# Performance work log

Measured on AMD Instinct MI355X. Metric: run time of the kernel, lower is better.

Reference implementation:

```python
import jax, jax.numpy as jnp
import numpy as np

B, N, D = 256, 64, 256   # graphs, nodes/graph, hidden dim (node_size*extend_dim)
T, E = B * N, 524288     # total nodes, total edges
NODE, BOND, K = 128, 16, 3
RRELU_SLOPE = (1.0 / 8.0 + 1.0 / 3.0) / 2.0  # eval-mode RReLU slope


def rrelu(x):
    return jnp.where(x >= 0, x, RRELU_SLOPE * x)


def conv_step(x, src, dst, ea, Wn, We, bm, Ws, bs):
    # message on each edge, scatter-add to destination, self-transform + update
    msg = jax.nn.relu(x[src] @ Wn + ea @ We + bm)          # [E, D]
    agg = jax.ops.segment_sum(msg, dst, num_segments=T)    # [T, D]
    return jax.nn.relu(x @ Ws + agg + bs)


def readout(x):
    # GlobalPool: cat([mean, sum, sort_pool(k=3)], -1) -> [B, 5D]
    xr = x.reshape(B, N, D)
    mean, s = xr.mean(1), xr.sum(1)
    order = jnp.argsort(-xr[..., -1], axis=1)[:, :K]                      # [B, K]
    topk = jnp.take_along_axis(xr, order[..., None], axis=1).reshape(B, K * D)
    return jnp.concatenate([mean, s, topk], -1)


def dot_pool(x1, x2):
    # per-graph cross-molecule dot product, max & mean -> [B, 2]
    item = jnp.einsum('bnd,bmd->bnm', x1.reshape(B, N, D), x2.reshape(B, N, D))
    return jnp.stack([item.max((1, 2)), item.mean((1, 2))], -1)


def setup_inputs() -> dict:
    key = jax.random.key(0)
    ks = jax.random.split(key, 32)
    batch = jnp.repeat(jnp.arange(B, dtype=jnp.int64), N)
    off = jnp.repeat(jnp.arange(B, dtype=jnp.int64) * N, E // B)

    def edges(k):
        s = jax.random.randint(k, (2, E), 0, N).astype(jnp.int64) + off[None, :]
        return s

    def w(k, shape):
        fan = shape[0]
        return jax.random.normal(k, shape, jnp.float32) * (1.0 / np.sqrt(fan))

    return {
        'x1': jax.random.normal(ks[0], (T, NODE), jnp.float32),
        'edge_index1': edges(ks[1]),
        'edge_attr1': jax.random.normal(ks[2], (E, BOND), jnp.float32),
        'batch1': batch,
        'x2': jax.random.normal(ks[3], (T, NODE), jnp.float32),
        'edge_index2': edges(ks[4]),
        'edge_attr2': jax.random.normal(ks[5], (E, BOND), jnp.float32),
        'batch2': batch,
        'W0_1': w(ks[6], (NODE, D)), 'b0_1': jnp.zeros(D),
        'W0_2': w(ks[7], (NODE, D)), 'b0_2': jnp.zeros(D),
        'Wn1': w(ks[8], (D, D)), 'We1': w(ks[9], (BOND, D)), 'bm1': jnp.zeros(D),
        'Ws1': w(ks[10], (D, D)), 'bs1': jnp.zeros(D),
        'Wn2': w(ks[11], (D, D)), 'We2': w(ks[12], (BOND, D)), 'bm2': jnp.zeros(D),
        'Ws2': w(ks[13], (D, D)), 'bs2': jnp.zeros(D),
        'Wf1': w(ks[14], (5 * D, D)), 'bf1': jnp.zeros(D),
        'Wf2': w(ks[15], (5 * D, D)), 'bf2': jnp.zeros(D),
        'Wo1': w(ks[16], (2 * D + 6, D)), 'bo1': jnp.zeros(D),
        'Wo2': w(ks[17], (D, 2)), 'bo2': jnp.zeros(2),
    }


def reference(x1, edge_index1, edge_attr1, batch1, x2, edge_index2, edge_attr2, batch2,
              W0_1, b0_1, W0_2, b0_2,
              Wn1, We1, bm1, Ws1, bs1,
              Wn2, We2, bm2, Ws2, bs2,
              Wf1, bf1, Wf2, bf2, Wo1, bo1, Wo2, bo2):
    xm1 = rrelu(x1 @ W0_1 + b0_1)
    xm2 = rrelu(x2 @ W0_2 + b0_2)
    s1, d1 = edge_index1[0], edge_index1[1]
    s2, d2 = edge_index2[0], edge_index2[1]
    fusion = []
    for _ in range(3):  # message_steps
        xm1 = conv_step(xm1, s1, d1, edge_attr1, Wn1, We1, bm1, Ws1, bs1)
        xm2 = conv_step(xm2, s2, d2, edge_attr2, Wn2, We2, bm2, Ws2, bs2)
        fusion.append(dot_pool(xm1, xm2))
    outm1 = readout(xm1) @ Wf1 + bf1
    outm2 = readout(xm2) @ Wf2 + bf2
    out = jnp.concatenate([outm1, outm2, jnp.concatenate(fusion, -1)], -1)
    out = out @ Wo1 + bo1
    return out @ Wo2 + bo2
```

## Files before the change

### kernel.cpp

```cpp
#include <hip/hip_runtime.h>
#include <hip/hip_fp16.h>

#define E_TOTAL 524288
#define RRELU_SLOPE 0.22916666666666666f

typedef float f32x4 __attribute__((ext_vector_type(4)));
typedef short short8_t __attribute__((ext_vector_type(8)));
typedef _Float16 half4_t __attribute__((ext_vector_type(4)));
typedef _Float16 h2v __attribute__((ext_vector_type(2)));

#define MFMA16F16 __builtin_amdgcn_mfma_f32_16x16x16f16

#if defined(__HIP_DEVICE_COMPILE__)
# if __has_builtin(__builtin_amdgcn_cvt_pkrtz)
#  define HAVE_PKRTZ 1
# endif
#endif

__device__ inline unsigned short f2bf(float x) {
  unsigned int u = __float_as_uint(x);
  u += 0x7FFFu + ((u >> 16) & 1u);
  return (unsigned short)(u >> 16);
}

__device__ inline unsigned int pack_h2(float a, float b) {
  __half2 h = __floats2half2_rn(a, b);
  return __builtin_bit_cast(unsigned int, h);
}

__device__ inline unsigned int pack_h2_fast(float a, float b) {
#ifdef HAVE_PKRTZ
  return __builtin_bit_cast(unsigned int, __builtin_amdgcn_cvt_pkrtz(a, b));
#else
  return pack_h2(a, b);
#endif
}

__global__ __launch_bounds__(256) void gemm_bf16_dual(
    const float* __restrict__ A1, const unsigned short* __restrict__ BT1,
    const float* __restrict__ bias1, float* __restrict__ C1,
    unsigned short* __restrict__ Ch1,
    const float* __restrict__ A2, const unsigned short* __restrict__ BT2,
    const float* __restrict__ bias2, float* __restrict__ C2,
    unsigned short* __restrict__ Ch2,
    int lda, int ldc, int K, int act)
{
  const float* A = blockIdx.z ? A2 : A1;
  const unsigned short* BT = blockIdx.z ? BT2 : BT1;
  const float* bias = blockIdx.z ? bias2 : bias1;
  float* C = blockIdx.z ? C2 : C1;
  unsigned short* Ch = blockIdx.z ? Ch2 : Ch1;

  __shared__ unsigned short As[128][32];
  __shared__ unsigned short Bs[128][32];
  const int tid = threadIdx.x;
  const int bm = blockIdx.x, bn = blockIdx.y;
  const int w = tid >> 6, l = tid & 63;
  const int wm = (w & 1) * 64, wn = (w >> 1) * 64;
  const int q = l >> 4, r = l & 15;

  f32x4 acc[4][4];
  for (int i = 0; i < 4; ++i)
    for (int j = 0; j < 4; ++j)
      acc[i][j] = (f32x4){0.f, 0.f, 0.f, 0.f};

  const int sm = tid >> 1;
  const int sk = (tid & 1) * 16;
  const float* ap = A + (size_t)(bm * 128 + sm) * lda + sk;
  const unsigned short* bp = BT + (size_t)(bn * 128 + sm) * K + sk;

  for (int k0 = 0; k0 < K; k0 += 32) {
    float4 f0 = *(const float4*)(ap + k0);
    float4 f1 = *(const float4*)(ap + k0 + 4);
    float4 f2 = *(const float4*)(ap + k0 + 8);
    float4 f3 = *(const float4*)(ap + k0 + 12);
    uint4 p0, p1;
    p0.x = (unsigned)f2bf(f0.x) | ((unsigned)f2bf(f0.y) << 16);
    p0.y = (unsigned)f2bf(f0.z) | ((unsigned)f2bf(f0.w) << 16);
    p0.z = (unsigned)f2bf(f1.x) | ((unsigned)f2bf(f1.y) << 16);
    p0.w = (unsigned)f2bf(f1.z) | ((unsigned)f2bf(f1.w) << 16);
    p1.x = (unsigned)f2bf(f2.x) | ((unsigned)f2bf(f2.y) << 16);
    p1.y = (unsigned)f2bf(f2.z) | ((unsigned)f2bf(f2.w) << 16);
    p1.z = (unsigned)f2bf(f3.x) | ((unsigned)f2bf(f3.y) << 16);
    p1.w = (unsigned)f2bf(f3.z) | ((unsigned)f2bf(f3.w) << 16);
    *(uint4*)&As[sm][sk] = p0;
    *(uint4*)&As[sm][sk + 8] = p1;
    uint4 b0 = *(const uint4*)(bp + k0);
    uint4 b1 = *(const uint4*)(bp + k0 + 8);
    *(uint4*)&Bs[sm][sk] = b0;
    *(uint4*)&Bs[sm][sk + 8] = b1;
    __syncthreads();

    short8_t af[4], bfr[4];
    for (int mt = 0; mt < 4; ++mt)
      af[mt] = *(const short8_t*)&As[wm + mt * 16 + r][q * 8];
    for (int nt = 0; nt < 4; ++nt)
      bfr[nt] = *(const short8_t*)&Bs[wn + nt * 16 + r][q * 8];
    for (int mt = 0; mt < 4; ++mt)
      for (int nt = 0; nt < 4; ++nt)
        acc[mt][nt] = __builtin_amdgcn_mfma_f32_16x16x32_bf16(
            af[mt], bfr[nt], acc[mt][nt], 0, 0, 0);
    __syncthreads();
  }

  for (int nt = 0; nt < 4; ++nt) {
    int gc = bn * 128 + wn + nt * 16 + r;
    float bv = bias ? bias[gc] : 0.f;
    for (int mt = 0; mt < 4; ++mt) {
      int gm = bm * 128 + wm + mt * 16 + q * 4;
      for (int rr = 0; rr < 4; ++rr) {
        float v = acc[mt][nt][rr] + bv;
        if (act == 2) v = (v >= 0.f) ? v : v * RRELU_SLOPE;
        if (Ch) Ch[(size_t)(gm + rr) * ldc + gc] = f2bf(v);
        else    C[(size_t)(gm + rr) * ldc + gc] = v;
      }
    }
  }
}

__global__ __launch_bounds__(256) void gemm_h_dual(
    const unsigned short* __restrict__ Ah1, const unsigned short* __restrict__ BT1,
    const float* __restrict__ bias1, float* __restrict__ C1,
    const unsigned short* __restrict__ Ah2, const unsigned short* __restrict__ BT2,
    const float* __restrict__ bias2, float* __restrict__ C2,
    int ldc, int K)
{
  const unsigned short* A = blockIdx.z ? Ah2 : Ah1;
  const unsigned short* BT = blockIdx.z ? BT2 : BT1;
  const float* bias = blockIdx.z ? bias2 : bias1;
  float* C = blockIdx.z ? C2 : C1;

  __shared__ unsigned short As[128][32];
  __shared__ unsigned short Bs[128][32];
  const int tid = threadIdx.x;
  const int bm = blockIdx.x, bn = blockIdx.y;
  const int w = tid >> 6, l = tid & 63;
  const int wm = (w & 1) * 64, wn = (w >> 1) * 64;
  const int q = l >> 4, r = l & 15;

  f32x4 acc[4][4];
  for (int i = 0; i < 4; ++i)
    for (int j = 0; j < 4; ++j)
      acc[i][j] = (f32x4){0.f, 0.f, 0.f, 0.f};

  const int sm = tid >> 1;
  const int sk = (tid & 1) * 16;
  const unsigned short* ap = A + (size_t)(bm * 128 + sm) * K + sk;
  const unsigned short* bp = BT + (size_t)(bn * 128 + sm) * K + sk;

  for (int k0 = 0; k0 < K; k0 += 32) {
    uint4 a0 = *(const uint4*)(ap + k0);
    uint4 a1 = *(const uint4*)(ap + k0 + 8);
    uint4 b0 = *(const uint4*)(bp + k0);
    uint4 b1 = *(const uint4*)(bp + k0 + 8);
    *(uint4*)&As[sm][sk] = a0;
    *(uint4*)&As[sm][sk + 8] = a1;
    *(uint4*)&Bs[sm][sk] = b0;
    *(uint4*)&Bs[sm][sk + 8] = b1;
    __syncthreads();

    short8_t af[4], bfr[4];
    for (int mt = 0; mt < 4; ++mt)
      af[mt] = *(const short8_t*)&As[wm + mt * 16 + r][q * 8];
    for (int nt = 0; nt < 4; ++nt)
      bfr[nt] = *(const short8_t*)&Bs[wn + nt * 16 + r][q * 8];
    for (int mt = 0; mt < 4; ++mt)
      for (int nt = 0; nt < 4; ++nt)
        acc[mt][nt] = __builtin_amdgcn_mfma_f32_16x16x32_bf16(
            af[mt], bfr[nt], acc[mt][nt], 0, 0, 0);
    __syncthreads();
  }

  for (int nt = 0; nt < 4; ++nt) {
    int gc = bn * 128 + wn + nt * 16 + r;
    float bv = bias ? bias[gc] : 0.f;
    for (int mt = 0; mt < 4; ++mt) {
      int gm = bm * 128 + wm + mt * 16 + q * 4;
      for (int rr = 0; rr < 4; ++rr)
        C[(size_t)(gm + rr) * ldc + gc] = acc[mt][nt][rr] + bv;
    }
  }
}

__global__ __launch_bounds__(256) void sort_edges_dual(
    const int* __restrict__ ei1, const int* __restrict__ ei2,
    int* __restrict__ meta1, int* __restrict__ meta2,
    int* __restrict__ perm1, int* __restrict__ perm2,
    int* __restrict__ starts1, int* __restrict__ starts2)
{
  const int mol = blockIdx.x >> 8;
  const int g = blockIdx.x & 255;
  const int* eidx = mol ? ei2 : ei1;
  int* meta = mol ? meta2 : meta1;
  int* perm = mol ? perm2 : perm1;
  int* starts = mol ? starts2 : starts1;

  __shared__ int cnt[4][64];
  __shared__ int startS[65];
  __shared__ int cur[64];
  const int t = threadIdx.x, w = t >> 6;
  cnt[w][t & 63] = 0;
  if (t < 64) cur[t] = 0;
  __syncthreads();
  for (int i = t; i < 2048; i += 256)
    atomicAdd(&cnt[w][eidx[E_TOTAL + g * 2048 + i] & 63], 1);
  __syncthreads();
  if (t == 0) {
    int acc = 0;
    for (int n = 0; n < 64; ++n) {
      startS[n] = acc;
      acc += cnt[0][n] + cnt[1][n] + cnt[2][n] + cnt[3][n];
    }
    startS[64] = acc;
  }
  __syncthreads();
  if (t < 65) starts[g * 65 + t] = startS[t];
  for (int i = t; i < 2048; i += 256) {
    int s = eidx[g * 2048 + i] & 63;
    int d = eidx[E_TOTAL + g * 2048 + i] & 63;
    int p = startS[d] + atomicAdd(&cur[d], 1);
    meta[g * 2048 + p] = s | (d << 8);
    perm[g * 2048 + p] = i;
  }
}

__global__ __launch_bounds__(256) void ea_gather_pack_dual(
    const float* __restrict__ ea1, const float* __restrict__ ea2,
    const int* __restrict__ perm1, const int* __restrict__ perm2,
    unsigned int* __restrict__ o1, unsigned int* __restrict__ o2)
{
  const int mol = blockIdx.x >> 11;
  const float* ea = mol ? ea2 : ea1;
  const int* perm = mol ? perm2 : perm1;
  unsigned int* out = mol ? o2 : o1;
  int p = (blockIdx.x & 2047) * 256 + threadIdx.x;
  int g = p >> 11;
  int i = perm[p];
  const float* s = ea + (size_t)(g * 2048 + i) * 16;
  float4 v0 = *(const float4*)(s);
  float4 v1 = *(const float4*)(s + 4);
  float4 v2 = *(const float4*)(s + 8);
  float4 v3 = *(const float4*)(s + 12);
  uint4 q0, q1;
  q0.x = pack_h2(v0.x, v0.y); q0.y = pack_h2(v0.z, v0.w);
  q0.z = pack_h2(v1.x, v1.y); q0.w = pack_h2(v1.z, v1.w);
  q1.x = pack_h2(v2.x, v2.y); q1.y = pack_h2(v2.z, v2.w);
  q1.z = pack_h2(v3.x, v3.y); q1.w = pack_h2(v3.z, v3.w);
  *(uint4*)(out + (size_t)p * 8) = q0;
  *(uint4*)(out + (size_t)p * 8 + 4) = q1;
}

__global__ __launch_bounds__(512, 4) void edge_conv_dual(
    const float* __restrict__ y1, const int* __restrict__ meta1,
    const unsigned int* __restrict__ eas1, const unsigned int* __restrict__ wep1,
    const int* __restrict__ st1, float* __restrict__ xo1,
    unsigned short* __restrict__ xoh1,
    const float* __restrict__ y2, const int* __restrict__ meta2,
    const unsigned int* __restrict__ eas2, const unsigned int* __restrict__ wep2,
    const int* __restrict__ st2, float* __restrict__ xo2,
    unsigned short* __restrict__ xoh2)
{
  const float* y; const int* meta; const unsigned int* eas;
  const unsigned int* wep; const int* st; float* xo; unsigned short* xoh;
  if (blockIdx.z == 0) { y = y1; meta = meta1; eas = eas1; wep = wep1; st = st1; xo = xo1; xoh = xoh1; }
  else                 { y = y2; meta = meta2; eas = eas2; wep = wep2; st = st2; xo = xo2; xoh = xoh2; }

  __shared__ unsigned int ypk[4160];
  const int g = blockIdx.x >> 1;
  const int dbase = (blockIdx.x & 1) * 128;
  const int tid = threadIdx.x;
  const int l = tid & 63;
  const int w = tid >> 6;
  const int rh = l & 15;
  const int qh = l >> 4;
  const int rhw = w * 8 + rh;

  for (int i = tid; i < 4096; i += 512) {
    int n = i >> 6, j = i & 63;
    const float* yr = y + (size_t)(g * 64 + n) * 512 + dbase + j;
    ypk[n * 65 + j] = pack_h2_fast(yr[0], yr[64]);
  }

  uint2 bfr[8];
#pragma unroll
  for (int c = 0; c < 8; ++c) {
    int d = dbase + c * 16 + rh;
    bfr[c].x = wep[(2 * qh) * 256 + d];
    bfr[c].y = wep[(2 * qh + 1) * 256 + d];
  }

  __syncthreads();

  const int estart = st[g * 65 + w * 8];
  const int eend   = st[g * 65 + w * 8 + 8];

  f32x4 acc[8];
#pragma unroll
  for (int i = 0; i < 8; ++i) acc[i] = (f32x4){0.f, 0.f, 0.f, 0.f};

  int base = estart;
  uint2 af = {0u, 0u};
  int mv = -1;
  if (base < eend) {
    int lim = eend - base; if (lim > 16) lim = 16;
    af = *(const uint2*)(eas + ((size_t)g * 2048 + base + (rh < lim ? rh : lim - 1)) * 8 + 2 * qh);
    int m = meta[(size_t)g * 2048 + base + (l < lim ? l : lim - 1)];
    mv = (l < lim) ? m : -1;
  }

  while (base < eend) {
    int mp[4];
#pragma unroll
    for (int v = 0; v < 4; ++v)
      mp[v] = __builtin_amdgcn_ds_bpermute(qh * 16 + v * 4, mv);

    int nbase = base + 16;
    uint2 afn = af;
    int mvn = -1;
    if (nbase < eend) {
      int nlim = eend - nbase; if (nlim > 16) nlim = 16;
      afn = *(const uint2*)(eas + ((size_t)g * 2048 + nbase + (rh < nlim ? rh : nlim - 1)) * 8 + 2 * qh);
      int m2 = meta[(size_t)g * 2048 + nbase + (l < nlim ? l : nlim - 1)];
      mvn = (l < nlim) ? m2 : -1;
    }

    half4_t afh = __builtin_bit_cast(half4_t, af);
    f32x4 pa[4], pb[4];
#pragma unroll
    for (int cp = 0; cp < 4; ++cp) {
      f32x4 z = (f32x4){0.f, 0.f, 0.f, 0.f};
      pa[cp] = MFMA16F16(afh, __builtin_bit_cast(half4_t, bfr[cp]), z, 0, 0, 0);
      pb[cp] = MFMA16F16(afh, __builtin_bit_cast(half4_t, bfr[cp + 4]), z, 0, 0, 0);
    }

    unsigned int yv[4][4];
    unsigned int ind[4];
#pragma unroll
    for (int v = 0; v < 4; ++v) {
      int sv = mp[v] & 63;
      int dv = (mp[v] >> 8) & 255;
      const unsigned int* yb = ypk + sv * 65 + rh;
      yv[0][v] = yb[0];
      yv[1][v] = yb[16];
      yv[2][v] = yb[32];
      yv[3][v] = yb[48];
      ind[v] = (dv == rhw) ? 0x3C00u : 0u;
    }
    uint2 su;
    su.x = ind[0] | (ind[1] << 16);
    su.y = ind[2] | (ind[3] << 16);
    half4_t sfrag = __builtin_bit_cast(half4_t, su);

    const h2v hz = {(_Float16)0.0f, (_Float16)0.0f};
#pragma unroll
    for (int cp = 0; cp < 4; ++cp) {
      unsigned int t[4];
#pragma unroll
      for (int v = 0; v < 4; ++v) {
        h2v s = __builtin_bit_cast(h2v, pack_h2_fast(pa[cp][v], pb[cp][v]));
        s = s + __builtin_bit_cast(h2v, yv[cp][v]);
        s = __builtin_elementwise_max(s, hz);
        t[v] = __builtin_bit_cast(unsigned int, s);
      }
      uint2 blo, bhi;
      blo.x = __builtin_amdgcn_perm(t[1], t[0], 0x05040100u);
      blo.y = __builtin_amdgcn_perm(t[3], t[2], 0x05040100u);
      bhi.x = __builtin_amdgcn_perm(t[1], t[0], 0x07060302u);
      bhi.y = __builtin_amdgcn_perm(t[3], t[2], 0x07060302u);
      acc[cp]     = MFMA16F16(sfrag, __builtin_bit_cast(half4_t, blo), acc[cp], 0, 0, 0);
      acc[cp + 4] = MFMA16F16(sfrag, __builtin_bit_cast(half4_t, bhi), acc[cp + 4], 0, 0, 0);
    }

    base = nbase;
    af = afn;
    mv = mvn;
  }

  if (qh < 2) {
#pragma unroll
    for (int v = 0; v < 4; ++v) {
      int node = g * 64 + w * 8 + qh * 4 + v;
      const float* ysp = y + (size_t)node * 512 + 256 + dbase + rh;
      float* xop = xo + (size_t)node * 256 + dbase + rh;
      unsigned short* xohp = xoh + (size_t)node * 256 + dbase + rh;
#pragma unroll
      for (int cp = 0; cp < 8; ++cp) {
        int dim = (cp & 3) * 16 + (cp >> 2) * 64;
        float val = fmaxf(ysp[dim] + acc[cp][v], 0.f);
        xop[dim] = val;
        xohp[dim] = f2bf(val);
      }
    }
  }
}

__global__ __launch_bounds__(256) void dot_pool_mfma(
    const unsigned short* __restrict__ x1h, const unsigned short* __restrict__ x2h,
    float* __restrict__ fusion, int step)
{
  __shared__ unsigned short s1[64][256];
  __shared__ unsigned short s2[64][256];
  const int g = blockIdx.x, tid = threadIdx.x;
  const int l = tid & 63, w = tid >> 6;
  const int r = l & 15, q = l >> 4;

  for (int i = tid; i < 2048; i += 256) {
    int row = i >> 5, c = i & 31;
    int cs = c ^ (row & 7);
    *(uint4*)&s1[row][cs * 8] = *(const uint4*)(x1h + (size_t)(g * 64 + row) * 256 + c * 8);
    *(uint4*)&s2[row][cs * 8] = *(const uint4*)(x2h + (size_t)(g * 64 + row) * 256 + c * 8);
  }
  __syncthreads();

  const int m0 = w * 16;
  const int sx = r & 7;
  f32x4 acc[4];
#pragma unroll
  for (int nt = 0; nt < 4; ++nt) acc[nt] = (f32x4){0.f, 0.f, 0.f, 0.f};

#pragma unroll
  for (int kb = 0; kb < 32; kb += 4) {
    int ch = (kb + q) ^ sx;
    short8_t af = *(const short8_t*)&s1[m0 + r][ch * 8];
#pragma unroll
    for (int nt = 0; nt < 4; ++nt) {
      short8_t bf = *(const short8_t*)&s2[nt * 16 + r][ch * 8];
      acc[nt] = __builtin_amdgcn_mfma_f32_16x16x32_bf16(af, bf, acc[nt], 0, 0, 0);
    }
  }

  float mymax = -1e30f, mysum = 0.f;
#pragma unroll
  for (int nt = 0; nt < 4; ++nt)
#pragma unroll
    for (int reg = 0; reg < 4; ++reg) {
      float v = acc[nt][reg];
      mymax = fmaxf(mymax, v);
      mysum += v;
    }
  for (int off = 32; off; off >>= 1) {
    mymax = fmaxf(mymax, __shfl_down(mymax, off, 64));
    mysum += __shfl_down(mysum, off, 64);
  }
  __syncthreads();
  float* red = (float*)&s1[0][0];
  if (l == 0) { red[w] = mymax; red[8 + w] = mysum; }
  __syncthreads();
  if (tid == 0) {
    float gm = fmaxf(fmaxf(red[0], red[1]), fmaxf(red[2], red[3]));
    float gs = red[8] + red[9] + red[10] + red[11];
    fusion[g * 6 + step * 2] = gm;
    fusion[g * 6 + step * 2 + 1] = gs * (1.f / 4096.f);
  }
}

__global__ __launch_bounds__(256) void readout_dual(
    const float* __restrict__ xm1, const float* __restrict__ xm2,
    float* __restrict__ R1, float* __restrict__ R2)
{
  const int mol = blockIdx.x >> 8;
  const float* xm = mol ? xm2 : xm1;
  float* R = mol ? R2 : R1;
  __shared__ float lastcol[64];
  __shared__ int topi[3];
  const int g = blockIdx.x & 255, d = threadIdx.x;
  float s = 0.f;
  for (int n = 0; n < 64; ++n) s += xm[(size_t)(g * 64 + n) * 256 + d];
  R[(size_t)g * 1280 + d] = s * (1.f / 64.f);
  R[(size_t)g * 1280 + 256 + d] = s;
  if (d < 64) lastcol[d] = xm[(size_t)(g * 64 + d) * 256 + 255];
  __syncthreads();
  if (d == 0) {
    unsigned long long used = 0;
    for (int j = 0; j < 3; ++j) {
      float best = -1e30f;
      int bi = 0;
      for (int n = 0; n < 64; ++n) {
        if ((used >> n) & 1ull) continue;
        if (lastcol[n] > best) { best = lastcol[n]; bi = n; }
      }
      used |= (1ull << bi);
      topi[j] = bi;
    }
  }
  __syncthreads();
  for (int j = 0; j < 3; ++j)
    R[(size_t)g * 1280 + 512 + j * 256 + d] =
        xm[(size_t)(g * 64 + topi[j]) * 256 + d];
}

__global__ __launch_bounds__(256) void final_head(
    const float* __restrict__ outm1, const float* __restrict__ outm2,
    const float* __restrict__ fusion,
    const float* __restrict__ Wo1, const float* __restrict__ bo1,
    const float* __restrict__ Wo2, const float* __restrict__ bo2,
    float* __restrict__ out)
{
  __shared__ float cat[520];
  __shared__ float r0s[4], r1s[4];
  const int g = blockIdx.x, t = threadIdx.x;
  cat[t] = outm1[(size_t)g * 256 + t];
  cat[256 + t] = outm2[(size_t)g * 256 + t];
  if (t < 6) cat[512 + t] = fusion[g * 6 + t];
  __syncthreads();
  float a0 = 0.f, a1 = 0.f, a2 = 0.f, a3 = 0.f;
  for (int k = 0; k < 516; k += 4) {
    a0 = fmaf(cat[k],     Wo1[(size_t)(k)     * 256 + t], a0);
    a1 = fmaf(cat[k + 1], Wo1[(size_t)(k + 1) * 256 + t], a1);
    a2 = fmaf(cat[k + 2], Wo1[(size_t)(k + 2) * 256 + t], a2);
    a3 = fmaf(cat[k + 3], Wo1[(size_t)(k + 3) * 256 + t], a3);
  }
  a0 = fmaf(cat[516], Wo1[(size_t)516 * 256 + t], a0);
  a1 = fmaf(cat[517], Wo1[(size_t)517 * 256 + t], a1);
  float acc = bo1[t] + ((a0 + a1) + (a2 + a3));
  float p0 = acc * Wo2[t * 2];
  float p1 = acc * Wo2[t * 2 + 1];
  for (int off = 32; off; off >>= 1) {
    p0 += __shfl_down(p0, off, 64);
    p1 += __shfl_down(p1, off, 64);
  }
  if ((t & 63) == 0) { r0s[t >> 6] = p0; r1s[t >> 6] = p1; }
  __syncthreads();
  if (t == 0) {
    out[g * 2] = r0s[0] + r0s[1] + r0s[2] + r0s[3] + bo2[0];
    out[g * 2 + 1] = r1s[0] + r1s[1] + r1s[2] + r1s[3] + bo2[1];
  }
}

__global__ __launch_bounds__(256) void transpose_all(
    const float* __restrict__ W0_1, const float* __restrict__ W0_2,
    const float* __restrict__ Wn1, const float* __restrict__ Ws1,
    const float* __restrict__ Wn2, const float* __restrict__ Ws2,
    const float* __restrict__ Wf1, const float* __restrict__ Wf2,
    unsigned short* __restrict__ W0T1, unsigned short* __restrict__ W0T2,
    unsigned short* __restrict__ WcT1, unsigned short* __restrict__ WcT2,
    unsigned short* __restrict__ WfT1, unsigned short* __restrict__ WfT2)
{
  const int b = blockIdx.x;
  const float* src; unsigned short* dst; int k0, K;
  if (b < 2)       { src = W0_1; dst = W0T1;         K = 128;  k0 = b * 64; }
  else if (b < 4)  { src = W0_2; dst = W0T2;         K = 128;  k0 = (b - 2) * 64; }
  else if (b < 8)  { src = Wn1;  dst = WcT1;         K = 256;  k0 = (b - 4) * 64; }
  else if (b < 12) { src = Ws1;  dst = WcT1 + 65536; K = 256;  k0 = (b - 8) * 64; }
  else if (b < 16) { src = Wn2;  dst = WcT2;         K = 256;  k0 = (b - 12) * 64; }
  else if (b < 20) { src = Ws2;  dst = WcT2 + 65536; K = 256;  k0 = (b - 16) * 64; }
  else if (b < 40) { src = Wf1;  dst = WfT1;         K = 1280; k0 = (b - 20) * 64; }
  else             { src = Wf2;  dst = WfT2;         K = 1280; k0 = (b - 40) * 64; }

  __shared__ unsigned short t[64][258];
  const int tid = threadIdx.x;
  for (int i = tid; i < 16384; i += 256) {
    int row = i >> 8, col = i & 255;
    t[row][col] = f2bf(src[(size_t)(k0 + row) * 256 + col]);
  }
  __syncthreads();
  unsigned short* dp = dst + (size_t)tid * K + k0;
  for (int k = 0; k < 64; k += 8) {
    uint4 v;
    v.x = (unsigned)t[k + 0][tid] | ((unsigned)t[k + 1][tid] << 16);
    v.y = (unsigned)t[k + 2][tid] | ((unsigned)t[k + 3][tid] << 16);
    v.z = (unsigned)t[k + 4][tid] | ((unsigned)t[k + 5][tid] << 16);
    v.w = (unsigned)t[k + 6][tid] | ((unsigned)t[k + 7][tid] << 16);
    *(uint4*)(dp + k) = v;
  }
}

__global__ void misc_prep(
    const float* bm1, const float* bs1, const float* bm2, const float* bs2,
    const float* We1, const float* We2,
    float* bcat1, float* bcat2,
    unsigned int* weh1, unsigned int* weh2)
{
  int idx = blockIdx.x * 256 + threadIdx.x;
  if (idx < 512) {
    bcat1[idx] = idx < 256 ? bm1[idx] : bs1[idx - 256];
  } else if (idx < 1024) {
    int i = idx - 512;
    bcat2[i] = i < 256 ? bm2[i] : bs2[i - 256];
  } else if (idx < 3072) {
    int i = idx - 1024, j = i >> 8, d = i & 255;
    weh1[i] = pack_h2(We1[(2 * j) * 256 + d], We1[(2 * j + 1) * 256 + d]);
  } else if (idx < 5120) {
    int i = idx - 3072, j = i >> 8, d = i & 255;
    weh2[i] = pack_h2(We2[(2 * j) * 256 + d], We2[(2 * j + 1) * 256 + d]);
  }
}

extern "C" void kernel_launch(void* const* d_in, const int* in_sizes, int n_in,
                              void* d_out, int out_size, void* d_ws, size_t ws_size,
                              hipStream_t stream)
{
  const float* x1 = (const float*)d_in[0];
  const int* ei1 = (const int*)d_in[1];
  const float* ea1 = (const float*)d_in[2];
  const float* x2 = (const float*)d_in[4];
  const int* ei2 = (const int*)d_in[5];
  const float* ea2 = (const float*)d_in[6];
  const float* W0_1 = (const float*)d_in[8];
  const float* b0_1 = (const float*)d_in[9];
  const float* W0_2 = (const float*)d_in[10];
  const float* b0_2 = (const float*)d_in[11];
  const float* Wn1 = (const float*)d_in[12];
  const float* We1 = (const float*)d_in[13];
  const float* bm1 = (const float*)d_in[14];
  const float* Ws1 = (const float*)d_in[15];
  const float* bs1 = (const float*)d_in[16];
  const float* Wn2 = (const float*)d_in[17];
  const float* We2 = (const float*)d_in[18];
  const float* bm2 = (const float*)d_in[19];
  const float* Ws2 = (const float*)d_in[20];
  const float* bs2 = (const float*)d_in[21];
  const float* Wf1 = (const float*)d_in[22];
  const float* bf1 = (const float*)d_in[23];
  const float* Wf2 = (const float*)d_in[24];
  const float* bf2 = (const float*)d_in[25];
  const float* Wo1 = (const float*)d_in[26];
  const float* bo1 = (const float*)d_in[27];
  const float* Wo2 = (const float*)d_in[28];
  const float* bo2 = (const float*)d_in[29];
  float* out = (float*)d_out;

  float* w = (float*)d_ws;
  size_t off = 0;
  auto alloc = [&](size_t nf) { float* p = w + off; off += nf; return p; };
  float* xmA1 = alloc(4194304);
  float* xmA2 = alloc(4194304);
  float* xmB1 = alloc(4194304);
  float* xmB2 = alloc(4194304);
  float* y1 = alloc(8388608);
  float* y2 = alloc(8388608);
  float* R1 = alloc(327680);
  float* R2 = alloc(327680);
  float* outm1 = alloc(65536);
  float* outm2 = alloc(65536);
  float* fusion = alloc(1536);
  float* bcat1 = alloc(512);
  float* bcat2 = alloc(512);
  unsigned short* W0T1 = (unsigned short*)alloc(16384);
  unsigned short* W0T2 = (unsigned short*)alloc(16384);
  unsigned short* WcT1 = (unsigned short*)alloc(65536);
  unsigned short* WcT2 = (unsigned short*)alloc(65536);
  unsigned short* WfT1 = (unsigned short*)alloc(163840);
  unsigned short* WfT2 = (unsigned short*)alloc(163840);
  unsigned int* weh1 = (unsigned int*)alloc(2048);
  unsigned int* weh2 = (unsigned int*)alloc(2048);
  unsigned int* eah1 = (unsigned int*)alloc(4194304);
  unsigned int* eah2 = (unsigned int*)alloc(4194304);
  int* meta1 = (int*)alloc(524288);
  int* meta2 = (int*)alloc(524288);
  int* perm1 = (int*)alloc(524288);
  int* perm2 = (int*)alloc(524288);
  int* starts1 = (int*)alloc(16640);
  int* starts2 = (int*)alloc(16640);
  unsigned short* xmhA1 = (unsigned short*)alloc(2097152);
  unsigned short* xmhA2 = (unsigned short*)alloc(2097152);
  unsigned short* xmhB1 = (unsigned short*)alloc(2097152);
  unsigned short* xmhB2 = (unsigned short*)alloc(2097152);
  (void)in_sizes; (void)n_in; (void)out_size; (void)ws_size;

  sort_edges_dual<<<512, 256, 0, stream>>>(ei1, ei2, meta1, meta2,
                                           perm1, perm2, starts1, starts2);
  transpose_all<<<60, 256, 0, stream>>>(W0_1, W0_2, Wn1, Ws1, Wn2, Ws2,
                                        Wf1, Wf2, W0T1, W0T2, WcT1, WcT2,
                                        WfT1, WfT2);
  misc_prep<<<20, 256, 0, stream>>>(bm1, bs1, bm2, bs2, We1, We2,
                                    bcat1, bcat2, weh1, weh2);
  ea_gather_pack_dual<<<4096, 256, 0, stream>>>(ea1, ea2, perm1, perm2,
                                                eah1, eah2);

  gemm_bf16_dual<<<dim3(128, 2, 2), 256, 0, stream>>>(
      x1, W0T1, b0_1, nullptr, xmhA1, x2, W0T2, b0_2, nullptr, xmhA2,
      128, 256, 128, 2);

  float* cur1 = xmA1; float* cur2 = xmA2;
  float* nxt1 = xmB1; float* nxt2 = xmB2;
  unsigned short* curh1 = xmhA1; unsigned short* curh2 = xmhA2;
  unsigned short* nxth1 = xmhB1; unsigned short* nxth2 = xmhB2;
  for (int step = 0; step < 3; ++step) {
    gemm_h_dual<<<dim3(128, 4, 2), 256, 0, stream>>>(
        curh1, WcT1, bcat1, y1, curh2, WcT2, bcat2, y2, 512, 256);
    edge_conv_dual<<<dim3(512, 1, 2), 512, 0, stream>>>(
        y1, meta1, eah1, weh1, starts1, nxt1, nxth1,
        y2, meta2, eah2, weh2, starts2, nxt2, nxth2);
    dot_pool_mfma<<<256, 256, 0, stream>>>(nxth1, nxth2, fusion, step);
    float* t1 = cur1; cur1 = nxt1; nxt1 = t1;
    float* t2 = cur2; cur2 = nxt2; nxt2 = t2;
    unsigned short* th1 = curh1; curh1 = nxth1; nxth1 = th1;
    unsigned short* th2 = curh2; curh2 = nxth2; nxth2 = th2;
  }

  readout_dual<<<512, 256, 0, stream>>>(cur1, cur2, R1, R2);
  gemm_bf16_dual<<<dim3(2, 2, 2), 256, 0, stream>>>(
      R1, WfT1, bf1, outm1, nullptr, R2, WfT2, bf2, outm2, nullptr,
      1280, 256, 1280, 0);
  final_head<<<256, 256, 0, stream>>>(outm1, outm2, fusion,
                                      Wo1, bo1, Wo2, bo2, out);
}
```

Baseline: 544.6 us.

## Split-K the readout projection GEMM and reduce partials in final head

Replaces the 8-block readout GEMM with a split-K kernel using 64x64 tiles over 10 K-chunks per molecule, producing partial sums. The final head kernel now sums the partials and adds the bias before its own matmul. This raises parallelism for a small-M GEMM that previously underfilled the GPU. The cost is extra partial-buffer traffic and redundant reduction work.

```diff
diff --git a/kernel.cpp b/kernel.cpp
--- a/kernel.cpp
+++ b/kernel.cpp
@@ -3,6 +3,7 @@
 
 #define E_TOTAL 524288
 #define RRELU_SLOPE 0.22916666666666666f
+#define NKSPLIT 10
 
 typedef float f32x4 __attribute__((ext_vector_type(4)));
 typedef short short8_t __attribute__((ext_vector_type(8)));
@@ -182,6 +183,71 @@
   }
 }
 
+__global__ __launch_bounds__(256) void gemm_splitk_dual(
+    const float* __restrict__ A1, const unsigned short* __restrict__ BT1,
+    float* __restrict__ P1,
+    const float* __restrict__ A2, const unsigned short* __restrict__ BT2,
+    float* __restrict__ P2)
+{
+  const int mol = blockIdx.z & 1;
+  const int kc = blockIdx.z >> 1;
+  const float* A = mol ? A2 : A1;
+  const unsigned short* BT = mol ? BT2 : BT1;
+  float* P = mol ? P2 : P1;
+  const int K = 1280;
+
+  __shared__ unsigned short As[64][32];
+  __shared__ unsigned short Bs[64][32];
+  const int tid = threadIdx.x;
+  const int m0 = blockIdx.x * 64, n0 = blockIdx.y * 64;
+  const int w = tid >> 6, l = tid & 63;
+  const int wm = (w & 1) * 32, wn = (w >> 1) * 32;
+  const int q = l >> 4, r = l & 15;
+
+  f32x4 acc[2][2];
+  for (int i = 0; i < 2; ++i)
+    for (int j = 0; j < 2; ++j)
+      acc[i][j] = (f32x4){0.f, 0.f, 0.f, 0.f};
+
+  const int sm = tid >> 2;
+  const int sk = (tid & 3) * 8;
+  const float* ap = A + (size_t)(m0 + sm) * K + kc * 128 + sk;
+  const unsigned short* bp = BT + (size_t)(n0 + sm) * K + kc * 128 + sk;
+
+  for (int k0 = 0; k0 < 128; k0 += 32) {
+    float4 f0 = *(const float4*)(ap + k0);
+    float4 f1 = *(const float4*)(ap + k0 + 4);
+    uint4 p0;
+    p0.x = (unsigned)f2bf(f0.x) | ((unsigned)f2bf(f0.y) << 16);
+    p0.y = (unsigned)f2bf(f0.z) | ((unsigned)f2bf(f0.w) << 16);
+    p0.z = (unsigned)f2bf(f1.x) | ((unsigned)f2bf(f1.y) << 16);
+    p0.w = (unsigned)f2bf(f1.z) | ((unsigned)f2bf(f1.w) << 16);
+    *(uint4*)&As[sm][sk] = p0;
+    *(uint4*)&Bs[sm][sk] = *(const uint4*)(bp + k0);
+    __syncthreads();
+
+    short8_t af[2], bfr[2];
+    for (int mt = 0; mt < 2; ++mt)
+      af[mt] = *(const short8_t*)&As[wm + mt * 16 + r][q * 8];
+    for (int nt = 0; nt < 2; ++nt)
+      bfr[nt] = *(const short8_t*)&Bs[wn + nt * 16 + r][q * 8];
+    for (int mt = 0; mt < 2; ++mt)
+      for (int nt = 0; nt < 2; ++nt)
+        acc[mt][nt] = __builtin_amdgcn_mfma_f32_16x16x32_bf16(
+            af[mt], bfr[nt], acc[mt][nt], 0, 0, 0);
+    __syncthreads();
+  }
+
+  for (int nt = 0; nt < 2; ++nt) {
+    int gc = n0 + wn + nt * 16 + r;
+    for (int mt = 0; mt < 2; ++mt) {
+      int gm = m0 + wm + mt * 16 + q * 4;
+      for (int rr = 0; rr < 4; ++rr)
+        P[((size_t)kc * 256 + gm + rr) * 256 + gc] = acc[mt][nt][rr];
+    }
+  }
+}
+
 __global__ __launch_bounds__(256) void sort_edges_dual(
     const int* __restrict__ ei1, const int* __restrict__ ei2,
     int* __restrict__ meta1, int* __restrict__ meta2,
@@ -490,7 +556,8 @@
 }
 
 __global__ __launch_bounds__(256) void final_head(
-    const float* __restrict__ outm1, const float* __restrict__ outm2,
+    const float* __restrict__ P1, const float* __restrict__ P2,
+    const float* __restrict__ bf1, const float* __restrict__ bf2,
     const float* __restrict__ fusion,
     const float* __restrict__ Wo1, const float* __restrict__ bo1,
     const float* __restrict__ Wo2, const float* __restrict__ bo2,
@@ -499,8 +566,14 @@
   __shared__ float cat[520];
   __shared__ float r0s[4], r1s[4];
   const int g = blockIdx.x, t = threadIdx.x;
-  cat[t] = outm1[(size_t)g * 256 + t];
-  cat[256 + t] = outm2[(size_t)g * 256 + t];
+  float s1 = bf1[t], s2 = bf2[t];
+#pragma unroll
+  for (int k = 0; k < NKSPLIT; ++k) {
+    s1 += P1[((size_t)k * 256 + g) * 256 + t];
+    s2 += P2[((size_t)k * 256 + g) * 256 + t];
+  }
+  cat[t] = s1;
+  cat[256 + t] = s2;
   if (t < 6) cat[512 + t] = fusion[g * 6 + t];
   __syncthreads();
   float a0 = 0.f, a1 = 0.f, a2 = 0.f, a3 = 0.f;
@@ -631,8 +704,8 @@
   float* y2 = alloc(8388608);
   float* R1 = alloc(327680);
   float* R2 = alloc(327680);
-  float* outm1 = alloc(65536);
-  float* outm2 = alloc(65536);
+  float* P1 = alloc(655360);
+  float* P2 = alloc(655360);
   float* fusion = alloc(1536);
   float* bcat1 = alloc(512);
   float* bcat2 = alloc(512);
@@ -690,9 +763,8 @@
   }
 
   readout_dual<<<512, 256, 0, stream>>>(cur1, cur2, R1, R2);
-  gemm_bf16_dual<<<dim3(2, 2, 2), 256, 0, stream>>>(
-      R1, WfT1, bf1, outm1, nullptr, R2, WfT2, bf2, outm2, nullptr,
-      1280, 256, 1280, 0);
-  final_head<<<256, 256, 0, stream>>>(outm1, outm2, fusion,
+  gemm_splitk_dual<<<dim3(4, 4, 2 * NKSPLIT), 256, 0, stream>>>(
+      R1, WfT1, P1, R2, WfT2, P2);
+  final_head<<<256, 256, 0, stream>>>(P1, P2, bf1, bf2, fusion,
                                       Wo1, bo1, Wo2, bo2, out);
 }
```

Result: faster. 497.1 us (-8.7%).
